# Optimization experiments

Hardware: AMD Instinct MI355X
Metric: run time of the kernel (lower is better)

The kernel has to match this reference:

```python
import jax, jax.numpy as jnp
import numpy as np
import math

B, S, D, H = 2, 2048, 1024, 16
DK = D // H


def setup_inputs() -> dict:
    key = jax.random.key(0)
    ks = jax.random.split(key, 11)
    s = 1.0 / math.sqrt(D)
    return {
        "q": jax.random.normal(ks[0], (B, S, D), jnp.float32),
        "k": jax.random.normal(ks[1], (B, S, D), jnp.float32),
        "v": jax.random.normal(ks[2], (B, S, D), jnp.float32),
        "Wq": jax.random.normal(ks[3], (D, D), jnp.float32) * s,
        "bq": jax.random.normal(ks[4], (D,), jnp.float32) * s,
        "Wk": jax.random.normal(ks[5], (D, D), jnp.float32) * s,
        "bk": jax.random.normal(ks[6], (D,), jnp.float32) * s,
        "Wv": jax.random.normal(ks[7], (D, D), jnp.float32) * s,
        "bv": jax.random.normal(ks[8], (D,), jnp.float32) * s,
        "Wo": jax.random.normal(ks[9], (D, D), jnp.float32) * s,
        "bo": jax.random.normal(ks[10], (D,), jnp.float32) * s,
    }


def reference(q, k, v, Wq, bq, Wk, bk, Wv, bv, Wo, bo):
    bs = q.shape[0]
    # linear projections, split heads: [B, H, S, DK]
    qh = (q @ Wq.T + bq).reshape(bs, -1, H, DK).transpose(0, 2, 1, 3)
    kh = (k @ Wk.T + bk).reshape(bs, -1, H, DK).transpose(0, 2, 1, 3)
    vh = (v @ Wv.T + bv).reshape(bs, -1, H, DK).transpose(0, 2, 1, 3)
    # scaled dot-product attention (dropout in eval mode -> identity)
    scores = jnp.einsum('bhqd,bhkd->bhqk', qh, kh) / math.sqrt(DK)
    attn = jax.nn.softmax(scores, axis=-1)
    out = jnp.einsum('bhqk,bhkd->bhqd', attn, vh)
    concat = out.transpose(0, 2, 1, 3).reshape(bs, -1, D)
    return concat @ Wo.T + bo
```

## Files before the change

### kernel.cpp

```cpp
#include <hip/hip_runtime.h>
#include <stdint.h>

#define DEV __device__ __forceinline__

typedef __bf16 bf16;
typedef __bf16 bf16x8 __attribute__((ext_vector_type(8)));
typedef unsigned short u16x8 __attribute__((ext_vector_type(8)));
typedef float f32x4 __attribute__((ext_vector_type(4)));
typedef uint32_t u32x4 __attribute__((ext_vector_type(4)));

static constexpr int S = 2048, D = 1024, NH = 16;
static constexpr float QSCALE = 0.125f * 1.44269504088896340736f;

union BU { u16x8 u; bf16x8 v; };
union PU { u32x4 u; bf16x8 v; };

DEV uint32_t pack2(float a, float b) {
  union { __bf16 h; uint16_t u; } x, y;
  x.h = (__bf16)a; y.h = (__bf16)b;
  return (uint32_t)x.u | ((uint32_t)y.u << 16);
}

struct CvtArgs { const float* s[7]; bf16* d[7]; };
__global__ __launch_bounds__(256) void cvt_all(CvtArgs a) {
  int blk = blockIdx.x, seg, rel;
  if (blk < 6144) { seg = blk >> 11; rel = blk & 2047; }
  else { int bb = blk - 6144; seg = 3 + (bb >> 9); rel = bb & 511; }
  int i = rel * 256 + threadIdx.x;
  const float4* p = (const float4*)a.s[seg] + (size_t)i * 2;
  float4 x = p[0], y = p[1];
  bf16x8 o;
  o[0] = (bf16)x.x; o[1] = (bf16)x.y; o[2] = (bf16)x.z; o[3] = (bf16)x.w;
  o[4] = (bf16)y.x; o[5] = (bf16)y.y; o[6] = (bf16)y.z; o[7] = (bf16)y.w;
  ((bf16x8*)a.d[seg])[i] = o;
}

DEV void async_copy16(bf16* lds_dst, const bf16* g_src) {
  __builtin_amdgcn_global_load_lds(
      (const __attribute__((address_space(1))) void*)(g_src),
      (__attribute__((address_space(3))) void*)(lds_dst),
      16, 0, 0);
}

struct GArgs {
  const bf16* A[3]; const bf16* W[3]; const float* bias[3];
  bf16* Cb[3]; float* Cf[3]; float scale[3];
};

template <bool OUT_F32>
__global__ __launch_bounds__(256, 2)
void gemm_multi(GArgs g) {
  constexpr int N = 1024, K = 1024;
  const int z = blockIdx.z;
  const bf16* A = g.A[z];
  const bf16* Bt = g.W[z];
  const float* bias = g.bias[z];
  const float scale = g.scale[z];

  __shared__ bf16 As[128 * 32];
  __shared__ bf16 Bs[128 * 32];
  const int t = threadIdx.x;
  const int w = t >> 6, l = t & 63;
  const int wr = w >> 1, wc = w & 1;
  const int lr = l & 15, lg = l >> 4;
  const int m0 = blockIdx.y * 128, n0 = blockIdx.x * 128;

  f32x4 acc[4][4] = {};

  const int srow = t >> 2, scol = (t & 3) * 8;
  const bf16* Aptr = A + (size_t)(m0 + srow) * K + scol;
  const bf16* Bptr = Bt + (size_t)(n0 + srow) * K + scol;
  bf16* AsDst = &As[w * 512];
  bf16* BsDst = &Bs[w * 512];

  for (int k0 = 0; k0 < K; k0 += 32) {
    async_copy16(AsDst,        Aptr + k0);
    async_copy16(AsDst + 2048, Aptr + (size_t)64 * K + k0);
    async_copy16(BsDst,        Bptr + k0);
    async_copy16(BsDst + 2048, Bptr + (size_t)64 * K + k0);
    __syncthreads();
    bf16x8 af[4], bfr[4];
#pragma unroll
    for (int i = 0; i < 4; i++)
      af[i] = *(const bf16x8*)&As[(wr * 64 + i * 16 + lr) * 32 + lg * 8];
#pragma unroll
    for (int i = 0; i < 4; i++)
      bfr[i] = *(const bf16x8*)&Bs[(wc * 64 + i * 16 + lr) * 32 + lg * 8];
#pragma unroll
    for (int mi = 0; mi < 4; mi++)
#pragma unroll
      for (int ni = 0; ni < 4; ni++)
        acc[mi][ni] = __builtin_amdgcn_mfma_f32_16x16x32_bf16(
            af[mi], bfr[ni], acc[mi][ni], 0, 0, 0);
    __syncthreads();
  }

#pragma unroll
  for (int mi = 0; mi < 4; mi++) {
#pragma unroll
    for (int ni = 0; ni < 4; ni++) {
      int col = n0 + wc * 64 + ni * 16 + lr;
      float bv = bias[col];
#pragma unroll
      for (int r = 0; r < 4; r++) {
        int row = m0 + wr * 64 + mi * 16 + lg * 4 + r;
        float v = (acc[mi][ni][r] + bv) * scale;
        if (OUT_F32) g.Cf[z][(size_t)row * N + col] = v;
        else         g.Cb[z][(size_t)row * N + col] = (bf16)v;
      }
    }
  }
}

__global__ __launch_bounds__(256, 2)
void attn_kernel(const bf16* __restrict__ Qp, const bf16* __restrict__ Kp,
                 const bf16* __restrict__ Vp, bf16* __restrict__ Oc) {
  __shared__ uint4 ldsu[1024];
  char* lds = (char*)ldsu;

  const int t = threadIdx.x, w = t >> 6, l = t & 63;
  const int lr = l & 15, lg = l >> 4;
  const int bh = blockIdx.y, b = bh >> 4, h = bh & 15;
  const int q0 = blockIdx.x * 128;
  const size_t base = (size_t)b * S * D + (size_t)h * 64;

  bf16x8 qf[2][2];
  {
    const bf16* qb = Qp + base + (size_t)(q0 + w * 32 + lr) * D + lg * 8;
#pragma unroll
    for (int qs = 0; qs < 2; qs++)
#pragma unroll
      for (int ks = 0; ks < 2; ks++)
        qf[qs][ks] = *(const bf16x8*)(qb + (size_t)qs * 16 * D + ks * 32);
  }

  f32x4 accO[2][4] = {};
  float mrun[2] = {-3e38f, -3e38f}, lrun[2] = {0.f, 0.f};

  const int srow = t >> 2, seg = t & 3;
  const int mm = (((srow >> 2) & 1) << 1) | (srow >> 5);
  const int rho = (mm << 4) | (((srow >> 3) & 3) << 2) | (srow & 3);
  const int kswz = (rho & 7) << 4;
  const int ka0 = (rho * 128 + seg * 32) ^ kswz;
  const int ka1 = (rho * 128 + seg * 32 + 16) ^ kswz;
  const int vu = t & 31, vc = t >> 5;
  const bf16* Kg = Kp + base + (size_t)srow * D + seg * 16;
  const bf16* Vg = Vp + base + (size_t)(2 * vu) * D + vc * 8;

  u16x8 k0 = *(const u16x8*)(Kg);
  u16x8 k1 = *(const u16x8*)(Kg + 8);
  u16x8 v0 = *(const u16x8*)(Vg);
  u16x8 v1 = *(const u16x8*)(Vg + D);

  const int rswz = (lr & 7) << 4;

  for (int kv0 = 0; kv0 < S; kv0 += 64) {
    __syncthreads();
    *(u16x8*)(lds + ka0) = k0;
    *(u16x8*)(lds + ka1) = k1;
#pragma unroll
    for (int j = 0; j < 8; j++) {
      uint32_t dw = (uint32_t)v0[j] | ((uint32_t)v1[j] << 16);
      int va = 8192 + ((((vc * 8 + j) * 128) + vu * 4) ^ (j << 4));
      *(uint32_t*)(lds + va) = dw;
    }
    __syncthreads();
    if (kv0 + 64 < S) {
      size_t off = (size_t)(kv0 + 64) * D;
      k0 = *(const u16x8*)(Kg + off);
      k1 = *(const u16x8*)(Kg + off + 8);
      v0 = *(const u16x8*)(Vg + off);
      v1 = *(const u16x8*)(Vg + off + D);
    }

    f32x4 sc[2][4] = {};
#pragma unroll
    for (int ks = 0; ks < 2; ks++) {
      BU kf[4];
#pragma unroll
      for (int m = 0; m < 4; m++)
        kf[m].u = *(const u16x8*)(lds + ((((m * 16 + lr) * 128) + ks * 64 + lg * 16) ^ rswz));
      __builtin_amdgcn_s_setprio(1);
#pragma unroll
      for (int m = 0; m < 4; m++)
#pragma unroll
        for (int qs = 0; qs < 2; qs++)
          sc[qs][m] = __builtin_amdgcn_mfma_f32_16x16x32_bf16(
              kf[m].v, qf[qs][ks], sc[qs][m], 0, 0, 0);
      __builtin_amdgcn_s_setprio(0);
    }

    uint32_t pk[2][4][2];
    float alq[2];
#pragma unroll
    for (int qs = 0; qs < 2; qs++) {
      float mx = sc[qs][0][0];
#pragma unroll
      for (int m = 0; m < 4; m++)
#pragma unroll
        for (int r = 0; r < 4; r++) mx = fmaxf(mx, sc[qs][m][r]);
      mx = fmaxf(mx, __shfl_xor(mx, 16));
      mx = fmaxf(mx, __shfl_xor(mx, 32));
      float mn = fmaxf(mrun[qs], mx);
      float al = exp2f(mrun[qs] - mn);
      mrun[qs] = mn;
      float s = 0.f;
#pragma unroll
      for (int m = 0; m < 4; m++) {
        float p0 = exp2f(sc[qs][m][0] - mn);
        float p1 = exp2f(sc[qs][m][1] - mn);
        float p2 = exp2f(sc[qs][m][2] - mn);
        float p3 = exp2f(sc[qs][m][3] - mn);
        s += (p0 + p1) + (p2 + p3);
        pk[qs][m][0] = pack2(p0, p1);
        pk[qs][m][1] = pack2(p2, p3);
      }
      s += __shfl_xor(s, 16);
      s += __shfl_xor(s, 32);
      lrun[qs] = lrun[qs] * al + s;
      alq[qs] = al;
    }
#pragma unroll
    for (int qs = 0; qs < 2; qs++)
#pragma unroll
      for (int r = 0; r < 4; r++) {
        float a = __shfl(alq[qs], (lg << 4) | (lg * 4 + r));
#pragma unroll
        for (int n = 0; n < 4; n++) accO[qs][n][r] *= a;
      }

#pragma unroll
    for (int ks = 0; ks < 2; ks++) {
      PU pa[2];
#pragma unroll
      for (int qs = 0; qs < 2; qs++) {
        pa[qs].u[0] = pk[qs][ks][0];
        pa[qs].u[1] = pk[qs][ks][1];
        pa[qs].u[2] = pk[qs][2 + ks][0];
        pa[qs].u[3] = pk[qs][2 + ks][1];
      }
      BU vf[4];
#pragma unroll
      for (int n = 0; n < 4; n++)
        vf[n].u = *(const u16x8*)(lds + 8192 +
                   ((((n * 16 + lr) * 128) + ks * 64 + lg * 16) ^ rswz));
      __builtin_amdgcn_s_setprio(1);
#pragma unroll
      for (int n = 0; n < 4; n++)
#pragma unroll
        for (int qs = 0; qs < 2; qs++)
          accO[qs][n] = __builtin_amdgcn_mfma_f32_16x16x32_bf16(
              pa[qs].v, vf[n].v, accO[qs][n], 0, 0, 0);
      __builtin_amdgcn_s_setprio(0);
    }
  }

#pragma unroll
  for (int qs = 0; qs < 2; qs++)
#pragma unroll
    for (int r = 0; r < 4; r++) {
      float lv = __shfl(lrun[qs], (lg << 4) | (lg * 4 + r));
      float rl = 1.0f / lv;
      int row = q0 + w * 32 + qs * 16 + lg * 4 + r;
      bf16* orow = Oc + base + (size_t)row * D;
#pragma unroll
      for (int n = 0; n < 4; n++) orow[n * 16 + lr] = (bf16)(accO[qs][n][r] * rl);
    }
}

extern "C" void kernel_launch(void* const* d_in, const int* in_sizes, int n_in,
                              void* d_out, int out_size, void* d_ws, size_t ws_size,
                              hipStream_t stream) {
  const float* q  = (const float*)d_in[0];
  const float* k  = (const float*)d_in[1];
  const float* v  = (const float*)d_in[2];
  const float* Wq = (const float*)d_in[3];
  const float* bq = (const float*)d_in[4];
  const float* Wk = (const float*)d_in[5];
  const float* bk = (const float*)d_in[6];
  const float* Wv = (const float*)d_in[7];
  const float* bv = (const float*)d_in[8];
  const float* Wo = (const float*)d_in[9];
  const float* bo = (const float*)d_in[10];
  float* out = (float*)d_out;

  const int BS = 2 * S;
  const size_t SZ_T = (size_t)BS * D * 2;
  const size_t SZ_W = (size_t)D * D * 2;

  char* ws = (char*)d_ws;
  bf16* qb  = (bf16*)(ws);
  bf16* kb  = (bf16*)(ws + SZ_T);
  bf16* vb  = (bf16*)(ws + 2 * SZ_T);
  bf16* Wqb = (bf16*)(ws + 3 * SZ_T);
  bf16* Wkb = (bf16*)(ws + 3 * SZ_T + SZ_W);
  bf16* Wvb = (bf16*)(ws + 3 * SZ_T + 2 * SZ_W);
  bf16* Wob = (bf16*)(ws + 3 * SZ_T + 3 * SZ_W);
  bf16* Qh  = (bf16*)(ws + 3 * SZ_T + 4 * SZ_W);
  bf16* Kh  = (bf16*)(ws + 4 * SZ_T + 4 * SZ_W);
  bf16* Vh  = (bf16*)(ws + 5 * SZ_T + 4 * SZ_W);
  bf16* Oc  = qb;

  CvtArgs ca;
  ca.s[0] = q;  ca.d[0] = qb;
  ca.s[1] = k;  ca.d[1] = kb;
  ca.s[2] = v;  ca.d[2] = vb;
  ca.s[3] = Wq; ca.d[3] = Wqb;
  ca.s[4] = Wk; ca.d[4] = Wkb;
  ca.s[5] = Wv; ca.d[5] = Wvb;
  ca.s[6] = Wo; ca.d[6] = Wob;
  cvt_all<<<dim3(8192), 256, 0, stream>>>(ca);

  GArgs gp = {};
  gp.A[0] = qb; gp.W[0] = Wqb; gp.bias[0] = bq; gp.Cb[0] = Qh; gp.scale[0] = QSCALE;
  gp.A[1] = kb; gp.W[1] = Wkb; gp.bias[1] = bk; gp.Cb[1] = Kh; gp.scale[1] = 1.0f;
  gp.A[2] = vb; gp.W[2] = Wvb; gp.bias[2] = bv; gp.Cb[2] = Vh; gp.scale[2] = 1.0f;
  gemm_multi<false><<<dim3(D / 128, BS / 128, 3), 256, 0, stream>>>(gp);

  attn_kernel<<<dim3(S / 128, 2 * NH), 256, 0, stream>>>(Qh, Kh, Vh, Oc);

  GArgs go = {};
  go.A[0] = Oc; go.W[0] = Wob; go.bias[0] = bo; go.Cf[0] = out; go.scale[0] = 1.0f;
  gemm_multi<true><<<dim3(D / 128, BS / 128, 1), 256, 0, stream>>>(go);
}
```

Baseline: 259.6 us.

## Double-buffer attention K/V tiles, lazy softmax rescale, and narrow GEMM tiles

Attention now double-buffers K and V in LDS, loading K with async copies and prefetching V two tiles ahead so each iteration needs a single barrier. Softmax skips the running-max rescale unless a row's max rises by more than a threshold, and defers the row-sum reduction to the end. The GEMMs switch to 128x64 tiles, doubling the block count for better occupancy on the projection and output GEMMs at the cost of less B-tile reuse. LDS use for attention doubles, and the lazy rescale risks exp2 overflow if scores grow past the threshold.

```diff
diff --git a/kernel.cpp b/kernel.cpp
--- a/kernel.cpp
+++ b/kernel.cpp
@@ -11,6 +11,7 @@
 
 static constexpr int S = 2048, D = 1024, NH = 16;
 static constexpr float QSCALE = 0.125f * 1.44269504088896340736f;
+static constexpr float DTHR = 8.0f;
 
 union BU { u16x8 u; bf16x8 v; };
 union PU { u32x4 u; bf16x8 v; };
@@ -58,14 +59,13 @@
   const float scale = g.scale[z];
 
   __shared__ bf16 As[128 * 32];
-  __shared__ bf16 Bs[128 * 32];
+  __shared__ bf16 Bs[64 * 32];
   const int t = threadIdx.x;
   const int w = t >> 6, l = t & 63;
-  const int wr = w >> 1, wc = w & 1;
   const int lr = l & 15, lg = l >> 4;
-  const int m0 = blockIdx.y * 128, n0 = blockIdx.x * 128;
-
-  f32x4 acc[4][4] = {};
+  const int m0 = blockIdx.y * 128, n0 = blockIdx.x * 64;
+
+  f32x4 acc[2][4] = {};
 
   const int srow = t >> 2, scol = (t & 3) * 8;
   const bf16* Aptr = A + (size_t)(m0 + srow) * K + scol;
@@ -77,17 +77,16 @@
     async_copy16(AsDst,        Aptr + k0);
     async_copy16(AsDst + 2048, Aptr + (size_t)64 * K + k0);
     async_copy16(BsDst,        Bptr + k0);
-    async_copy16(BsDst + 2048, Bptr + (size_t)64 * K + k0);
     __syncthreads();
-    bf16x8 af[4], bfr[4];
-#pragma unroll
-    for (int i = 0; i < 4; i++)
-      af[i] = *(const bf16x8*)&As[(wr * 64 + i * 16 + lr) * 32 + lg * 8];
-#pragma unroll
-    for (int i = 0; i < 4; i++)
-      bfr[i] = *(const bf16x8*)&Bs[(wc * 64 + i * 16 + lr) * 32 + lg * 8];
-#pragma unroll
-    for (int mi = 0; mi < 4; mi++)
+    bf16x8 af[2], bfr[4];
+#pragma unroll
+    for (int i = 0; i < 2; i++)
+      af[i] = *(const bf16x8*)&As[(w * 32 + i * 16 + lr) * 32 + lg * 8];
+#pragma unroll
+    for (int n = 0; n < 4; n++)
+      bfr[n] = *(const bf16x8*)&Bs[(n * 16 + lr) * 32 + lg * 8];
+#pragma unroll
+    for (int mi = 0; mi < 2; mi++)
 #pragma unroll
       for (int ni = 0; ni < 4; ni++)
         acc[mi][ni] = __builtin_amdgcn_mfma_f32_16x16x32_bf16(
@@ -96,14 +95,14 @@
   }
 
 #pragma unroll
-  for (int mi = 0; mi < 4; mi++) {
+  for (int mi = 0; mi < 2; mi++) {
 #pragma unroll
     for (int ni = 0; ni < 4; ni++) {
-      int col = n0 + wc * 64 + ni * 16 + lr;
+      int col = n0 + ni * 16 + lr;
       float bv = bias[col];
 #pragma unroll
       for (int r = 0; r < 4; r++) {
-        int row = m0 + wr * 64 + mi * 16 + lg * 4 + r;
+        int row = m0 + w * 32 + mi * 16 + lg * 4 + r;
         float v = (acc[mi][ni][r] + bv) * scale;
         if (OUT_F32) g.Cf[z][(size_t)row * N + col] = v;
         else         g.Cb[z][(size_t)row * N + col] = (bf16)v;
@@ -115,7 +114,7 @@
 __global__ __launch_bounds__(256, 2)
 void attn_kernel(const bf16* __restrict__ Qp, const bf16* __restrict__ Kp,
                  const bf16* __restrict__ Vp, bf16* __restrict__ Oc) {
-  __shared__ uint4 ldsu[1024];
+  __shared__ uint4 ldsu[2048];
   char* lds = (char*)ldsu;
 
   const int t = threadIdx.x, w = t >> 6, l = t & 63;
@@ -123,6 +122,7 @@
   const int bh = blockIdx.y, b = bh >> 4, h = bh & 15;
   const int q0 = blockIdx.x * 128;
   const size_t base = (size_t)b * S * D + (size_t)h * 64;
+  const size_t TILE = (size_t)64 * D;
 
   bf16x8 qf[2][2];
   {
@@ -135,43 +135,62 @@
   }
 
   f32x4 accO[2][4] = {};
-  float mrun[2] = {-3e38f, -3e38f}, lrun[2] = {0.f, 0.f};
-
-  const int srow = t >> 2, seg = t & 3;
-  const int mm = (((srow >> 2) & 1) << 1) | (srow >> 5);
-  const int rho = (mm << 4) | (((srow >> 3) & 3) << 2) | (srow & 3);
-  const int kswz = (rho & 7) << 4;
-  const int ka0 = (rho * 128 + seg * 32) ^ kswz;
-  const int ka1 = (rho * 128 + seg * 32 + 16) ^ kswz;
+  float mrun[2] = {-1e30f, -1e30f}, lsum[2] = {0.f, 0.f};
+
+  const bf16* kptr[2];
+#pragma unroll
+  for (int c = 0; c < 2; c++) {
+    int o = w * 2048 + c * 1024 + l * 16;
+    int rho = o >> 7;
+    int seg16 = ((o & 127) ^ ((rho & 7) << 4)) >> 4;
+    int mm = rho >> 4;
+    int srow = ((mm & 1) << 5) | (((rho >> 2) & 3) << 3) | ((mm >> 1) << 2) | (rho & 3);
+    kptr[c] = Kp + base + (size_t)srow * D + seg16 * 8;
+  }
+
   const int vu = t & 31, vc = t >> 5;
-  const bf16* Kg = Kp + base + (size_t)srow * D + seg * 16;
   const bf16* Vg = Vp + base + (size_t)(2 * vu) * D + vc * 8;
-
-  u16x8 k0 = *(const u16x8*)(Kg);
-  u16x8 k1 = *(const u16x8*)(Kg + 8);
-  u16x8 v0 = *(const u16x8*)(Vg);
-  u16x8 v1 = *(const u16x8*)(Vg + D);
+  int vwa[8];
+#pragma unroll
+  for (int j = 0; j < 8; j++)
+    vwa[j] = 16384 + (((vc * 8 + j) * 128 + vu * 4) ^ (j << 4));
 
   const int rswz = (lr & 7) << 4;
 
-  for (int kv0 = 0; kv0 < S; kv0 += 64) {
-    __syncthreads();
-    *(u16x8*)(lds + ka0) = k0;
-    *(u16x8*)(lds + ka1) = k1;
+  async_copy16((bf16*)(lds + w * 2048),        kptr[0]);
+  async_copy16((bf16*)(lds + w * 2048 + 1024), kptr[1]);
+  u16x8 va = *(const u16x8*)(Vg);
+  u16x8 vb = *(const u16x8*)(Vg + D);
+  __syncthreads();
+  {
 #pragma unroll
     for (int j = 0; j < 8; j++) {
-      uint32_t dw = (uint32_t)v0[j] | ((uint32_t)v1[j] << 16);
-      int va = 8192 + ((((vc * 8 + j) * 128) + vu * 4) ^ (j << 4));
-      *(uint32_t*)(lds + va) = dw;
-    }
-    __syncthreads();
-    if (kv0 + 64 < S) {
-      size_t off = (size_t)(kv0 + 64) * D;
-      k0 = *(const u16x8*)(Kg + off);
-      k1 = *(const u16x8*)(Kg + off + 8);
-      v0 = *(const u16x8*)(Vg + off);
-      v1 = *(const u16x8*)(Vg + off + D);
-    }
+      uint32_t dw = (uint32_t)va[j] | ((uint32_t)vb[j] << 16);
+      *(uint32_t*)(lds + vwa[j]) = dw;
+    }
+  }
+  va = *(const u16x8*)(Vg + TILE);
+  vb = *(const u16x8*)(Vg + TILE + D);
+  __syncthreads();
+
+  const bf16* kp0 = kptr[0] + TILE;
+  const bf16* kp1 = kptr[1] + TILE;
+  const bf16* vg2 = Vg + 2 * TILE;
+
+  for (int it = 0; it < 32; ++it) {
+    const int cur = (it & 1) * 8192;
+    const int nxt = ((it + 1) & 1) * 8192;
+    const bool hasN = it < 31, hasN2 = it < 30;
+
+    if (hasN) {
+      async_copy16((bf16*)(lds + nxt + w * 2048),        kp0);
+      async_copy16((bf16*)(lds + nxt + w * 2048 + 1024), kp1);
+      kp0 += TILE; kp1 += TILE;
+    }
+    const bf16* pv = hasN2 ? vg2 : (Vp + base);
+    u16x8 ta = *(const u16x8*)(pv);
+    u16x8 tb = *(const u16x8*)(pv + D);
+    vg2 += TILE;
 
     f32x4 sc[2][4] = {};
 #pragma unroll
@@ -179,7 +198,8 @@
       BU kf[4];
 #pragma unroll
       for (int m = 0; m < 4; m++)
-        kf[m].u = *(const u16x8*)(lds + ((((m * 16 + lr) * 128) + ks * 64 + lg * 16) ^ rswz));
+        kf[m].u = *(const u16x8*)(lds + cur +
+                   ((((m * 16 + lr) * 128) + ks * 64 + lg * 16) ^ rswz));
       __builtin_amdgcn_s_setprio(1);
 #pragma unroll
       for (int m = 0; m < 4; m++)
@@ -190,44 +210,61 @@
       __builtin_amdgcn_s_setprio(0);
     }
 
+    float mx[2];
+#pragma unroll
+    for (int qs = 0; qs < 2; qs++) {
+      float a0 = fmaxf(fmaxf(sc[qs][0][0], sc[qs][0][1]), fmaxf(sc[qs][0][2], sc[qs][0][3]));
+      float a1 = fmaxf(fmaxf(sc[qs][1][0], sc[qs][1][1]), fmaxf(sc[qs][1][2], sc[qs][1][3]));
+      float a2 = fmaxf(fmaxf(sc[qs][2][0], sc[qs][2][1]), fmaxf(sc[qs][2][2], sc[qs][2][3]));
+      float a3 = fmaxf(fmaxf(sc[qs][3][0], sc[qs][3][1]), fmaxf(sc[qs][3][2], sc[qs][3][3]));
+      mx[qs] = fmaxf(fmaxf(a0, a1), fmaxf(a2, a3));
+    }
+    bool stable = (mx[0] <= mrun[0] + DTHR) & (mx[1] <= mrun[1] + DTHR);
+    if (!__all(stable)) {
+      float alq[2];
+#pragma unroll
+      for (int qs = 0; qs < 2; qs++) {
+        float m2 = fmaxf(mx[qs], __shfl_xor(mx[qs], 16));
+        m2 = fmaxf(m2, __shfl_xor(m2, 32));
+        float mn = fmaxf(mrun[qs], m2);
+        float al = exp2f(mrun[qs] - mn);
+        mrun[qs] = mn;
+        lsum[qs] *= al;
+        alq[qs] = al;
+      }
+#pragma unroll
+      for (int qs = 0; qs < 2; qs++)
+#pragma unroll
+        for (int r = 0; r < 4; r++) {
+          float a = __shfl(alq[qs], (lg << 4) | (lg * 4 + r));
+#pragma unroll
+          for (int n = 0; n < 4; n++) accO[qs][n][r] *= a;
+        }
+    }
     uint32_t pk[2][4][2];
-    float alq[2];
 #pragma unroll
     for (int qs = 0; qs < 2; qs++) {
-      float mx = sc[qs][0][0];
-#pragma unroll
-      for (int m = 0; m < 4; m++)
-#pragma unroll
-        for (int r = 0; r < 4; r++) mx = fmaxf(mx, sc[qs][m][r]);
-      mx = fmaxf(mx, __shfl_xor(mx, 16));
-      mx = fmaxf(mx, __shfl_xor(mx, 32));
-      float mn = fmaxf(mrun[qs], mx);
-      float al = exp2f(mrun[qs] - mn);
-      mrun[qs] = mn;
       float s = 0.f;
 #pragma unroll
       for (int m = 0; m < 4; m++) {
-        float p0 = exp2f(sc[qs][m][0] - mn);
-        float p1 = exp2f(sc[qs][m][1] - mn);
-        float p2 = exp2f(sc[qs][m][2] - mn);
-        float p3 = exp2f(sc[qs][m][3] - mn);
+        float p0 = exp2f(sc[qs][m][0] - mrun[qs]);
+        float p1 = exp2f(sc[qs][m][1] - mrun[qs]);
+        float p2 = exp2f(sc[qs][m][2] - mrun[qs]);
+        float p3 = exp2f(sc[qs][m][3] - mrun[qs]);
         s += (p0 + p1) + (p2 + p3);
         pk[qs][m][0] = pack2(p0, p1);
         pk[qs][m][1] = pack2(p2, p3);
       }
-      s += __shfl_xor(s, 16);
-      s += __shfl_xor(s, 32);
-      lrun[qs] = lrun[qs] * al + s;
-      alq[qs] = al;
-    }
-#pragma unroll
-    for (int qs = 0; qs < 2; qs++)
-#pragma unroll
-      for (int r = 0; r < 4; r++) {
-        float a = __shfl(alq[qs], (lg << 4) | (lg * 4 + r));
-#pragma unroll
-        for (int n = 0; n < 4; n++) accO[qs][n][r] *= a;
-      }
+      lsum[qs] += s;
+    }
+
+    if (hasN) {
+#pragma unroll
+      for (int j = 0; j < 8; j++) {
+        uint32_t dw = (uint32_t)va[j] | ((uint32_t)vb[j] << 16);
+        *(uint32_t*)(lds + vwa[j] + nxt) = dw;
+      }
+    }
 
 #pragma unroll
     for (int ks = 0; ks < 2; ks++) {
@@ -242,7 +279,7 @@
       BU vf[4];
 #pragma unroll
       for (int n = 0; n < 4; n++)
-        vf[n].u = *(const u16x8*)(lds + 8192 +
+        vf[n].u = *(const u16x8*)(lds + 16384 + cur +
                    ((((n * 16 + lr) * 128) + ks * 64 + lg * 16) ^ rswz));
       __builtin_amdgcn_s_setprio(1);
 #pragma unroll
@@ -253,13 +290,21 @@
               pa[qs].v, vf[n].v, accO[qs][n], 0, 0, 0);
       __builtin_amdgcn_s_setprio(0);
     }
-  }
-
+
+    va = ta; vb = tb;
+    __syncthreads();
+  }
+
+#pragma unroll
+  for (int qs = 0; qs < 2; qs++) {
+    lsum[qs] += __shfl_xor(lsum[qs], 16);
+    lsum[qs] += __shfl_xor(lsum[qs], 32);
+  }
 #pragma unroll
   for (int qs = 0; qs < 2; qs++)
 #pragma unroll
     for (int r = 0; r < 4; r++) {
-      float lv = __shfl(lrun[qs], (lg << 4) | (lg * 4 + r));
+      float lv = __shfl(lsum[qs], (lg << 4) | (lg * 4 + r));
       float rl = 1.0f / lv;
       int row = q0 + w * 32 + qs * 16 + lg * 4 + r;
       bf16* orow = Oc + base + (size_t)row * D;
@@ -315,11 +360,11 @@
   gp.A[0] = qb; gp.W[0] = Wqb; gp.bias[0] = bq; gp.Cb[0] = Qh; gp.scale[0] = QSCALE;
   gp.A[1] = kb; gp.W[1] = Wkb; gp.bias[1] = bk; gp.Cb[1] = Kh; gp.scale[1] = 1.0f;
   gp.A[2] = vb; gp.W[2] = Wvb; gp.bias[2] = bv; gp.Cb[2] = Vh; gp.scale[2] = 1.0f;
-  gemm_multi<false><<<dim3(D / 128, BS / 128, 3), 256, 0, stream>>>(gp);
+  gemm_multi<false><<<dim3(D / 64, BS / 128, 3), 256, 0, stream>>>(gp);
 
   attn_kernel<<<dim3(S / 128, 2 * NH), 256, 0, stream>>>(Qh, Kh, Vh, Oc);
 
   GArgs go = {};
   go.A[0] = Oc; go.W[0] = Wob; go.bias[0] = bo; go.Cf[0] = out; go.scale[0] = 1.0f;
-  gemm_multi<true><<<dim3(D / 128, BS / 128, 1), 256, 0, stream>>>(go);
-}
+  gemm_multi<true><<<dim3(D / 64, BS / 128, 1), 256, 0, stream>>>(go);
+}
```

Result: faster. 253.5 us (-2.3%).
